# Kernel tuning notes

Hardware: AMD Instinct MI355X
Metric: run time of the kernel (lower is better)

Reference implementation:

```python
import jax, jax.numpy as jnp
import numpy as np

N = 50000      # nodes
E = 800000     # edges (avg degree 16)
LM = 768       # lm_input_dim
H = 192        # hidden_dim = 32*6
B6 = 32        # per-branch dim = hidden_dim/6
SLOPE = 0.01   # nn.LeakyReLU default negative slope


def setup_inputs() -> dict:
    key = jax.random.key(0)
    ks = jax.random.split(key, 32)
    f = lambda i, shape, s=0.05: (jax.random.normal(ks[i], shape, jnp.float32) * s)
    inp = {
        "pre_x": f(0, (N, LM)),
        "x": f(1, (N, LM)),
        "edge_index": jax.random.randint(ks[2], (2, E), 0, N),
        "edge_type": jax.random.randint(ks[3], (E,), 0, 3),
        "num_prop": f(4, (N, 5)),
        "num_category": f(5, (N, 1)),
        "des_tensor": f(6, (N, LM)),
        "tweet_tensor": f(7, (N, LM)),
        # parameters (torch nn.Linear convention: W is [out, in], y = x @ W.T + b)
        "W_des": f(8, (B6, LM)), "b_des": f(9, (B6,)),
        "W_tweet": f(10, (B6, LM)), "b_tweet": f(11, (B6,)),
        "W_tweet_tr": f(12, (B6, LM)), "b_tweet_tr": f(13, (B6,)),
        "W_prop": f(14, (B6, 5)), "b_prop": f(15, (B6,)),
        "W_cat": f(16, (B6, 1)), "b_cat": f(17, (B6,)),
        "W_text": f(18, (B6, LM)), "b_text": f(19, (B6,)),
        "W_in": f(20, (H, H)), "b_in": f(21, (H,)),
        "W_c1": f(22, (H, H)), "b_c1": f(23, (H,)),
        "W_c2": f(24, (H, H)), "b_c2": f(25, (H,)),
        "W_o1": f(26, (96, H)), "b_o1": f(27, (96,)),
        "W_o2": f(28, (2, 96)), "b_o2": f(29, (2,)),
    }
    return inp


def _gcn_conv(h, W, b, src, dst):
    """PyG GCNConv: symmetric-normalized aggregation with added self-loops.
    out[v] = sum_{u->v} (d_u d_v)^{-1/2} (h_u W^T) + (1/d_v) (h_v W^T) + b
    where d includes the self-loop (+1)."""
    n = h.shape[0]
    hW = h @ W.T                                                  # [N, H]
    deg = jax.ops.segment_sum(jnp.ones(src.shape[0], h.dtype), dst,
                              num_segments=n) + 1.0               # [N]
    dinv = jax.lax.rsqrt(deg)
    norm = dinv[src] * dinv[dst]                                  # [E]
    agg = jax.ops.segment_sum(hW[src] * norm[:, None], dst,
                              num_segments=n)                     # [N, H]
    return agg + hW * (1.0 / deg)[:, None] + b


def reference(pre_x, x, edge_index, edge_type, num_prop, num_category,
              des_tensor, tweet_tensor,
              W_des, b_des, W_tweet, b_tweet, W_tweet_tr, b_tweet_tr,
              W_prop, b_prop, W_cat, b_cat, W_text, b_text,
              W_in, b_in, W_c1, b_c1, W_c2, b_c2,
              W_o1, b_o1, W_o2, b_o2):
    lrelu = lambda v: jax.nn.leaky_relu(v, SLOPE)
    branch = lambda t, W, b: lrelu(t @ W.T + b)   # dropout is identity in eval

    d = branch(des_tensor, W_des, b_des)
    pre_t = branch(pre_x, W_tweet, b_tweet)
    t = branch(x, W_tweet_tr, b_tweet_tr)
    n = branch(num_prop, W_prop, b_prop)
    c = branch(num_category, W_cat, b_cat)
    tw = branch(tweet_tensor, W_text, b_text)

    h = jnp.concatenate((n, c, d, tw, pre_t, t), axis=1)          # [N, 192]
    h = lrelu(h @ W_in.T + b_in)

    src, dst = edge_index[0], edge_index[1]
    h = _gcn_conv(h, W_c1, b_c1, src, dst)
    h = _gcn_conv(h, W_c2, b_c2, src, dst)

    em = lrelu(h @ W_o1.T + b_o1)                                 # [N, 96]
    out = em @ W_o2.T + b_o2                                      # [N, 2]
    return (out, em)
```

## Files before the change

### kernel.cpp

```cpp
#include <hip/hip_runtime.h>

#define NN 50000
#define EE 800000
#define LMD 768
#define HD 192
#define SLOPE 0.01f

typedef short bf16x8 __attribute__((ext_vector_type(8)));
typedef float f32x4 __attribute__((ext_vector_type(4)));
typedef unsigned short u16;

__device__ __forceinline__ float lrelu(float v){ return v > 0.f ? v : SLOPE * v; }

__device__ __forceinline__ u16 f2bf(float f){
    unsigned u = __float_as_uint(f);
    u += 0x7FFF + ((u >> 16) & 1u);
    return (u16)(u >> 16);
}
__device__ __forceinline__ float bf2f(u16 v){
    return __uint_as_float(((unsigned)v) << 16);
}
__device__ __forceinline__ bf16x8 as_bf8(float4 v){
    union { float4 f; bf16x8 b; } u; u.f = v; return u.b;
}

__global__ __launch_bounds__(256) void k_prep(
    const float* __restrict__ W0, const float* __restrict__ W1,
    const float* __restrict__ W2, const float* __restrict__ W3,
    const float* __restrict__ Win, const float* __restrict__ Wc1,
    const float* __restrict__ Wc2, const float* __restrict__ Wo1,
    u16* __restrict__ out)
{
    int m = blockIdx.y;
    int idx = blockIdx.x * 256 + threadIdx.x;
    const float* src; int nelem; int K;
    switch (m) {
      case 0: src = W0;  nelem = 32*768;  K = 768; break;
      case 1: src = W1;  nelem = 32*768;  K = 768; break;
      case 2: src = W2;  nelem = 32*768;  K = 768; break;
      case 3: src = W3;  nelem = 32*768;  K = 768; break;
      case 4: src = Win; nelem = 192*192; K = 192; break;
      case 5: src = Wc1; nelem = 192*192; K = 192; break;
      case 6: src = Wc2; nelem = 192*192; K = 192; break;
      default: src = Wo1; nelem = 96*192; K = 192; break;
    }
    if (idx >= nelem) return;
    u16 v = f2bf(src[idx]);
    int c = idx / K, k = idx - c * K;
    int cb = c >> 4, lr = c & 15;
    int sg = k >> 5, kk = k & 31, hi = kk >> 3, j = kk & 7;
    int lane = hi * 16 + lr;
    size_t dst;
    if (m < 4)      dst = (size_t)m * 24576 + (sg * 2 + cb) * 512 + lane * 8 + j;
    else if (m < 7) dst = 98304 + (size_t)(m - 4) * 36864 + (sg * 12 + cb) * 512 + lane * 8 + j;
    else            dst = 208896 + (size_t)(sg * 6 + cb) * 512 + lane * 8 + j;
    out[dst] = v;
}

__global__ __launch_bounds__(256, 3) void k_branch(
    const float* __restrict__ des, const float* __restrict__ twt,
    const float* __restrict__ prex, const float* __restrict__ xx,
    const u16* __restrict__ Wf,
    const float* __restrict__ bd, const float* __restrict__ btx,
    const float* __restrict__ btw, const float* __restrict__ btr,
    u16* __restrict__ h)
{
    __shared__ u16 Abuf[16][776];
    __shared__ float scr[4][16][32];

    const int br = blockIdx.y;
    const float* A; const float* bias; int colBase;
    switch (br) {
      case 0:  A = des;  bias = bd;  colBase = 64;  break;
      case 1:  A = twt;  bias = btx; colBase = 96;  break;
      case 2:  A = prex; bias = btw; colBase = 128; break;
      default: A = xx;   bias = btr; colBase = 160; break;
    }

    const int t0 = threadIdx.x, w = t0 >> 6, l = t0 & 63;
    const int hi = l >> 4, lr = l & 15;

    bf16x8 Bfr[12];
    {
        const u16* wp = Wf + br * 24576;
        #pragma unroll
        for (int cc = 0; cc < 6; ++cc)
            #pragma unroll
            for (int cb = 0; cb < 2; ++cb)
                Bfr[cc * 2 + cb] = *(const bf16x8*)(wp + ((w * 6 + cc) * 2 + cb) * 512 + l * 8);
    }

    const int rrow = t0 >> 4;
    const int col0 = (t0 & 15) * 2;
    const float bias0 = bias[col0], bias1 = bias[col0 + 1];

    float4 f4[12];
    int tile = blockIdx.x;
    {
        const float* ab = A + (size_t)tile * 12288 + w * 3072 + l * 4;
        #pragma unroll
        for (int i = 0; i < 12; ++i) f4[i] = *(const float4*)(ab + i * 256);
    }

    for (; tile < 3125; tile += 192) {
        asm volatile("s_waitcnt vmcnt(0)" ::: "memory");
        #pragma unroll
        for (int i = 0; i < 12; ++i) {
            const int rr = i / 3, third = i % 3;
            uint2 pk;
            pk.x = (unsigned)f2bf(f4[i].x) | ((unsigned)f2bf(f4[i].y) << 16);
            pk.y = (unsigned)f2bf(f4[i].z) | ((unsigned)f2bf(f4[i].w) << 16);
            *(uint2*)&Abuf[w * 4 + rr][third * 256 + l * 4] = pk;
        }
        const int tnext = tile + 192;
        if (tnext < 3125) {
            const float* ab = A + (size_t)tnext * 12288 + w * 3072 + l * 4;
            #pragma unroll
            for (int i = 0; i < 12; ++i) f4[i] = *(const float4*)(ab + i * 256);
        }
        __syncthreads();

        f32x4 acc[2] = {};
        #pragma unroll
        for (int cc = 0; cc < 6; ++cc) {
            const int cg = w * 6 + cc;
            bf16x8 af = *(const bf16x8*)&Abuf[lr][cg * 32 + hi * 8];
            acc[0] = __builtin_amdgcn_mfma_f32_16x16x32_bf16(af, Bfr[cc * 2 + 0], acc[0], 0, 0, 0);
            acc[1] = __builtin_amdgcn_mfma_f32_16x16x32_bf16(af, Bfr[cc * 2 + 1], acc[1], 0, 0, 0);
        }
        #pragma unroll
        for (int cb = 0; cb < 2; ++cb)
            #pragma unroll
            for (int rg = 0; rg < 4; ++rg)
                scr[w][hi * 4 + rg][cb * 16 + lr] = acc[cb][rg];
        __syncthreads();

        float2 s; s.x = 0.f; s.y = 0.f;
        #pragma unroll
        for (int ww = 0; ww < 4; ++ww) {
            float2 p = *(const float2*)&scr[ww][rrow][col0];
            s.x += p.x; s.y += p.y;
        }
        unsigned pk = (unsigned)f2bf(lrelu(s.x + bias0)) | ((unsigned)f2bf(lrelu(s.y + bias1)) << 16);
        *(unsigned*)&h[((size_t)tile * 16 + rrow) * HD + colBase + col0] = pk;
    }
}

__global__ __launch_bounds__(256) void k_small_branch(
    const float* __restrict__ nprop, const float* __restrict__ ncat,
    const float* __restrict__ Wp, const float* __restrict__ bp,
    const float* __restrict__ Wc, const float* __restrict__ bc,
    u16* __restrict__ h)
{
    __shared__ float sWp[160], sbp[32], sWc[32], sbc[32];
    int t = threadIdx.x;
    if (t < 160) sWp[t] = Wp[t];
    else if (t < 192) sbp[t - 160] = bp[t - 160];
    else if (t < 224) sWc[t - 192] = Wc[t - 192];
    else              sbc[t - 224] = bc[t - 224];
    __syncthreads();

    int idx = blockIdx.x * 256 + t;
    if (idx >= NN * 8) return;
    int row = idx >> 3, g = idx & 7;
    float o[8];
    if (g < 4) {
        float np[5];
        #pragma unroll
        for (int k = 0; k < 5; ++k) np[k] = nprop[row * 5 + k];
        #pragma unroll
        for (int j = 0; j < 8; ++j) {
            int c = g * 8 + j;
            float a = sbp[c];
            #pragma unroll
            for (int k = 0; k < 5; ++k) a += np[k] * sWp[c * 5 + k];
            o[j] = lrelu(a);
        }
    } else {
        float nc = ncat[row];
        #pragma unroll
        for (int j = 0; j < 8; ++j) {
            int cc = (g - 4) * 8 + j;
            o[j] = lrelu(sbc[cc] + nc * sWc[cc]);
        }
    }
    uint4 pk;
    pk.x = (unsigned)f2bf(o[0]) | ((unsigned)f2bf(o[1]) << 16);
    pk.y = (unsigned)f2bf(o[2]) | ((unsigned)f2bf(o[3]) << 16);
    pk.z = (unsigned)f2bf(o[4]) | ((unsigned)f2bf(o[5]) << 16);
    pk.w = (unsigned)f2bf(o[6]) | ((unsigned)f2bf(o[7]) << 16);
    *(uint4*)&h[(size_t)row * HD + g * 8] = pk;
}

template<bool BIAS, bool LRELU>
__global__ __launch_bounds__(512) void k_hgemm(
    const u16* __restrict__ A, const u16* __restrict__ Wf,
    const float* __restrict__ bias, u16* __restrict__ out)
{
    __shared__ u16 Bs[36864];
    const int t = threadIdx.x, w = t >> 6, l = t & 63;
    const int hi = l >> 4, lr = l & 15;
    const int rowBase = blockIdx.x * 128;
    {
        const uint4* s_ = (const uint4*)Wf; uint4* d_ = (uint4*)Bs;
        #pragma unroll
        for (int i = 0; i < 9; ++i) d_[i * 512 + t] = s_[i * 512 + t];
    }
    int r0 = rowBase + w * 16 + lr;
    int rowc = r0 < NN ? r0 : NN - 1;
    const u16* ap = A + (size_t)rowc * HD;
    float4 araw[6];
    #pragma unroll
    for (int sg = 0; sg < 6; ++sg) {
        araw[sg] = *(const float4*)(ap + sg * 32 + hi * 8);
        asm volatile("" :: "v"(araw[sg].x), "v"(araw[sg].y), "v"(araw[sg].z), "v"(araw[sg].w));
    }
    __syncthreads();

    f32x4 acc[12] = {};
    #pragma unroll
    for (int sg = 0; sg < 6; ++sg) {
        bf16x8 af = as_bf8(araw[sg]);
        #pragma unroll
        for (int cb = 0; cb < 12; ++cb) {
            bf16x8 bf = *(const bf16x8*)(Bs + (sg * 12 + cb) * 512 + l * 8);
            acc[cb] = __builtin_amdgcn_mfma_f32_16x16x32_bf16(af, bf, acc[cb], 0, 0, 0);
        }
    }

    #pragma unroll
    for (int cb = 0; cb < 12; ++cb) {
        int cl = cb * 16 + lr;
        float bv = BIAS ? bias[cl] : 0.f;
        #pragma unroll
        for (int rg = 0; rg < 4; ++rg) {
            int r = rowBase + w * 16 + hi * 4 + rg;
            if (r < NN) {
                float v = acc[cb][rg] + bv;
                if (LRELU) v = lrelu(v);
                out[(size_t)r * HD + cl] = f2bf(v);
            }
        }
    }
}

__global__ __launch_bounds__(512) void k_final(
    const u16* __restrict__ A, const u16* __restrict__ Wf,
    const float* __restrict__ b1, const float* __restrict__ W2,
    const float* __restrict__ b2, float* __restrict__ em, float* __restrict__ out)
{
    __shared__ u16 Bs[18432];
    const int t = threadIdx.x, w = t >> 6, l = t & 63;
    const int hi = l >> 4, lr = l & 15;
    const int rowBase = blockIdx.x * 128;
    {
        const uint4* s_ = (const uint4*)Wf; uint4* d_ = (uint4*)Bs;
        #pragma unroll
        for (int i = 0; i < 5; ++i) { int idx = i * 512 + t; if (idx < 2304) d_[idx] = s_[idx]; }
    }
    int r0 = rowBase + w * 16 + lr;
    int rowc = r0 < NN ? r0 : NN - 1;
    const u16* ap = A + (size_t)rowc * HD;
    float4 araw[6];
    #pragma unroll
    for (int sg = 0; sg < 6; ++sg) {
        araw[sg] = *(const float4*)(ap + sg * 32 + hi * 8);
        asm volatile("" :: "v"(araw[sg].x), "v"(araw[sg].y), "v"(araw[sg].z), "v"(araw[sg].w));
    }
    __syncthreads();

    f32x4 acc[6] = {};
    #pragma unroll
    for (int sg = 0; sg < 6; ++sg) {
        bf16x8 af = as_bf8(araw[sg]);
        #pragma unroll
        for (int cb = 0; cb < 6; ++cb) {
            bf16x8 bf = *(const bf16x8*)(Bs + (sg * 6 + cb) * 512 + l * 8);
            acc[cb] = __builtin_amdgcn_mfma_f32_16x16x32_bf16(af, bf, acc[cb], 0, 0, 0);
        }
    }

    float w2v[2][6], bv[6];
    #pragma unroll
    for (int cb = 0; cb < 6; ++cb) {
        bv[cb] = b1[cb * 16 + lr];
        w2v[0][cb] = W2[cb * 16 + lr];
        w2v[1][cb] = W2[96 + cb * 16 + lr];
    }

    #pragma unroll
    for (int rg = 0; rg < 4; ++rg) {
        int r = rowBase + w * 16 + hi * 4 + rg;
        float o0 = 0.f, o1 = 0.f;
        #pragma unroll
        for (int cb = 0; cb < 6; ++cb) {
            float v = lrelu(acc[cb][rg] + bv[cb]);
            if (r < NN) em[(size_t)r * 96 + cb * 16 + lr] = v;
            o0 += v * w2v[0][cb];
            o1 += v * w2v[1][cb];
        }
        #pragma unroll
        for (int d = 1; d < 16; d <<= 1) {
            o0 += __shfl_xor(o0, d);
            o1 += __shfl_xor(o1, d);
        }
        if (lr == 0 && r < NN) {
            out[r * 2 + 0] = o0 + b2[0];
            out[r * 2 + 1] = o1 + b2[1];
        }
    }
}

__global__ void k_count(const int* __restrict__ ei, int* __restrict__ deg)
{
    int e = blockIdx.x * 256 + threadIdx.x;
    if (e < EE) atomicAdd(&deg[ei[EE + e]], 1);
}

__global__ __launch_bounds__(1024) void k_scan1(const int* __restrict__ deg, int* __restrict__ rp,
                                                int* __restrict__ part,
                                                float* __restrict__ dinv, float* __restrict__ invdeg)
{
    __shared__ int sh[1024];
    int tid = threadIdx.x, i = blockIdx.x * 1024 + tid;
    int x = (i < NN) ? deg[i] : 0;
    if (i < NN) {
        float d = (float)(x + 1);
        dinv[i] = rsqrtf(d);
        invdeg[i] = 1.0f / d;
    }
    sh[tid] = x;
    __syncthreads();
    for (int off = 1; off < 1024; off <<= 1) {
        int y = (tid >= off) ? sh[tid - off] : 0;
        __syncthreads();
        sh[tid] += y;
        __syncthreads();
    }
    if (i < NN) rp[i] = sh[tid] - x;
    if (tid == 1023) part[blockIdx.x] = sh[tid];
}

__global__ void k_scan3(const int* __restrict__ deg, int* __restrict__ rp,
                        const int* __restrict__ part, int* __restrict__ cursor)
{
    int i = blockIdx.x * 256 + threadIdx.x;
    int pb = blockIdx.x >> 2;
    int pre = 0;
    for (int j = 0; j < pb; ++j) pre += part[j];
    if (i < NN) {
        int v = rp[i] + pre;
        rp[i] = v;
        cursor[i] = v;
        if (i == NN - 1) rp[NN] = v + deg[i];
    }
}

__global__ void k_fill(const int* __restrict__ ei, const float* __restrict__ dinv,
                       int* __restrict__ cursor, int* __restrict__ cs, float* __restrict__ nrm)
{
    int e = blockIdx.x * 256 + threadIdx.x;
    if (e >= EE) return;
    int s = ei[e], d = ei[EE + e];
    int pos = atomicAdd(&cursor[d], 1);
    cs[pos] = s;
    nrm[pos] = dinv[s] * dinv[d];
}

__global__ __launch_bounds__(256) void k_agg(const u16* __restrict__ hW,
    const int* __restrict__ rp, const int* __restrict__ cs, const float* __restrict__ nrm,
    const float* __restrict__ invdeg, const float* __restrict__ bias, u16* __restrict__ out)
{
    int lane = threadIdx.x;
    if (lane >= 48) return;
    int v = blockIdx.x * 4 + threadIdx.y;
    int f0 = lane * 4;
    int s0 = rp[v], s1 = rp[v + 1];
    float4 bv = *reinterpret_cast<const float4*>(bias + f0);
    ushort4 hv = *reinterpret_cast<const ushort4*>(hW + (size_t)v * HD + f0);
    float idg = invdeg[v];
    float a0 = bf2f(hv.x) * idg + bv.x;
    float a1 = bf2f(hv.y) * idg + bv.y;
    float a2 = bf2f(hv.z) * idg + bv.z;
    float a3 = bf2f(hv.w) * idg + bv.w;
    int i = s0;
    for (; i + 8 <= s1; i += 8) {
        int c[8]; float n[8]; ushort4 g[8];
        #pragma unroll
        for (int j = 0; j < 8; ++j) { c[j] = cs[i + j]; n[j] = nrm[i + j]; }
        #pragma unroll
        for (int j = 0; j < 8; ++j)
            g[j] = *reinterpret_cast<const ushort4*>(hW + (size_t)c[j] * HD + f0);
        #pragma unroll
        for (int j = 0; j < 8; ++j) {
            a0 += bf2f(g[j].x) * n[j]; a1 += bf2f(g[j].y) * n[j];
            a2 += bf2f(g[j].z) * n[j]; a3 += bf2f(g[j].w) * n[j];
        }
    }
    for (; i < s1; ++i) {
        int c = cs[i]; float n = nrm[i];
        ushort4 g = *reinterpret_cast<const ushort4*>(hW + (size_t)c * HD + f0);
        a0 += bf2f(g.x) * n; a1 += bf2f(g.y) * n; a2 += bf2f(g.z) * n; a3 += bf2f(g.w) * n;
    }
    ushort4 o;
    o.x = f2bf(a0); o.y = f2bf(a1); o.z = f2bf(a2); o.w = f2bf(a3);
    *reinterpret_cast<ushort4*>(out + (size_t)v * HD + f0) = o;
}

extern "C" void kernel_launch(void* const* d_in, const int* in_sizes, int n_in,
                              void* d_out, int out_size, void* d_ws, size_t ws_size,
                              hipStream_t stream)
{
    const float* pre_x = (const float*)d_in[0];
    const float* x     = (const float*)d_in[1];
    const int*   ei    = (const int*)d_in[2];
    const float* nprop = (const float*)d_in[4];
    const float* ncat  = (const float*)d_in[5];
    const float* des   = (const float*)d_in[6];
    const float* twt   = (const float*)d_in[7];
    const float* W_des  = (const float*)d_in[8],  *b_des  = (const float*)d_in[9];
    const float* W_tw   = (const float*)d_in[10], *b_tw   = (const float*)d_in[11];
    const float* W_tr   = (const float*)d_in[12], *b_tr   = (const float*)d_in[13];
    const float* W_prop = (const float*)d_in[14], *b_prop = (const float*)d_in[15];
    const float* W_cat  = (const float*)d_in[16], *b_cat  = (const float*)d_in[17];
    const float* W_text = (const float*)d_in[18], *b_text = (const float*)d_in[19];
    const float* W_in   = (const float*)d_in[20], *b_in   = (const float*)d_in[21];
    const float* W_c1   = (const float*)d_in[22], *b_c1   = (const float*)d_in[23];
    const float* W_c2   = (const float*)d_in[24], *b_c2   = (const float*)d_in[25];
    const float* W_o1   = (const float*)d_in[26], *b_o1   = (const float*)d_in[27];
    const float* W_o2   = (const float*)d_in[28], *b_o2   = (const float*)d_in[29];

    char* base = (char*)d_ws;
    size_t off = 0;
    auto alloc = [&](size_t bytes) -> char* {
        char* p = base + off;
        off = (off + bytes + 255) & ~(size_t)255;
        return p;
    };
    u16*   hA     = (u16*)alloc((size_t)NN * HD * 2);
    u16*   hB     = (u16*)alloc((size_t)NN * HD * 2);
    u16*   hC     = (u16*)alloc((size_t)NN * HD * 2);
    u16*   Wprep  = (u16*)alloc((size_t)227328 * 2);
    float* dinv   = (float*)alloc((size_t)NN * 4);
    float* invdeg = (float*)alloc((size_t)NN * 4);
    int*   deg    = (int*)alloc((size_t)NN * 4);
    int*   rp     = (int*)alloc((size_t)(NN + 1) * 4);
    int*   cursor = (int*)alloc((size_t)NN * 4);
    int*   part   = (int*)alloc(64 * 4);
    int*   cs     = (int*)alloc((size_t)EE * 4);
    float* nrm    = (float*)alloc((size_t)EE * 4);
    (void)ws_size; (void)in_sizes; (void)n_in; (void)out_size;

    float* outp = (float*)d_out;
    float* em   = outp + (size_t)NN * 2;

    const int rb     = (NN + 255) / 256;
    const int rb128  = (NN + 127) / 128;
    const int eb     = (EE + 255) / 256;
    const int nb1024 = (NN + 1023) / 1024;

    hipMemsetAsync(deg, 0, (size_t)NN * 4, stream);
    hipLaunchKernelGGL(k_prep, dim3(144, 8), dim3(256), 0, stream,
        W_des, W_text, W_tw, W_tr, W_in, W_c1, W_c2, W_o1, Wprep);
    hipLaunchKernelGGL(k_count,  dim3(eb), dim3(256), 0, stream, ei, deg);
    hipLaunchKernelGGL(k_scan1,  dim3(nb1024), dim3(1024), 0, stream, deg, rp, part, dinv, invdeg);
    hipLaunchKernelGGL(k_scan3,  dim3(rb), dim3(256), 0, stream, deg, rp, part, cursor);
    hipLaunchKernelGGL(k_fill,   dim3(eb), dim3(256), 0, stream, ei, dinv, cursor, cs, nrm);

    hipLaunchKernelGGL(k_branch, dim3(192, 4), dim3(256), 0, stream,
        des, twt, pre_x, x, Wprep, b_des, b_text, b_tw, b_tr, hA);
    hipLaunchKernelGGL(k_small_branch, dim3((NN * 8 + 255) / 256), dim3(256), 0, stream,
        nprop, ncat, W_prop, b_prop, W_cat, b_cat, hA);

    hipLaunchKernelGGL((k_hgemm<true, true>),   dim3(rb128), dim3(512), 0, stream,
        hA, Wprep + 98304, b_in, hB);
    hipLaunchKernelGGL((k_hgemm<false, false>), dim3(rb128), dim3(512), 0, stream,
        hB, Wprep + 98304 + 36864, nullptr, hC);
    hipLaunchKernelGGL(k_agg, dim3(NN / 4), dim3(64, 4), 0, stream, hC, rp, cs, nrm, invdeg, b_c1, hB);
    hipLaunchKernelGGL((k_hgemm<false, false>), dim3(rb128), dim3(512), 0, stream,
        hB, Wprep + 98304 + 2 * 36864, nullptr, hC);
    hipLaunchKernelGGL(k_agg, dim3(NN / 4), dim3(64, 4), 0, stream, hC, rp, cs, nrm, invdeg, b_c2, hB);

    hipLaunchKernelGGL(k_final, dim3(rb128), dim3(512), 0, stream,
        hB, Wprep + 208896, b_o1, W_o2, b_o2, em, outp);
}
```

Baseline: 400.8 us.

## Fold CSR graph build into compute kernels as extra blocks

The separate degree-count, scan and fill kernels are removed, and their work is given to extra blocks appended to the branch GEMM, the small-branch kernel and the first two hidden GEMMs. Graph preprocessing therefore runs alongside dense compute with fewer kernel launches. The branch GEMM also switches from strided tile assignment to contiguous tile ranges per block. In exchange, the scan uses 256-wide partials with a serial prefix over up to 196 parts, and the atomic-heavy blocks compete with the GEMM blocks for compute units.

```diff
diff --git a/kernel.cpp b/kernel.cpp
--- a/kernel.cpp
+++ b/kernel.cpp
@@ -63,10 +63,18 @@
     const u16* __restrict__ Wf,
     const float* __restrict__ bd, const float* __restrict__ btx,
     const float* __restrict__ btw, const float* __restrict__ btr,
-    u16* __restrict__ h)
+    u16* __restrict__ h,
+    const int* __restrict__ ei, int* __restrict__ deg)
 {
     __shared__ u16 Abuf[16][776];
     __shared__ float scr[4][16][32];
+
+    if (blockIdx.x >= 192) {
+        int rid = blockIdx.y * 64 + (blockIdx.x - 192);
+        for (int e = rid * 256 + threadIdx.x; e < EE; e += 65536)
+            atomicAdd(&deg[ei[EE + e]], 1);
+        return;
+    }
 
     const int br = blockIdx.y;
     const float* A; const float* bias; int colBase;
@@ -94,15 +102,18 @@
     const int col0 = (t0 & 15) * 2;
     const float bias0 = bias[col0], bias1 = bias[col0 + 1];
 
+    const int b = blockIdx.x;
+    const int nt = (b < 53) ? 17 : 16;
+    int tile = b * 16 + (b < 53 ? b : 53);
+
     float4 f4[12];
-    int tile = blockIdx.x;
     {
         const float* ab = A + (size_t)tile * 12288 + w * 3072 + l * 4;
         #pragma unroll
         for (int i = 0; i < 12; ++i) f4[i] = *(const float4*)(ab + i * 256);
     }
 
-    for (; tile < 3125; tile += 192) {
+    for (int it = 0; it < nt; ++it, ++tile) {
         asm volatile("s_waitcnt vmcnt(0)" ::: "memory");
         #pragma unroll
         for (int i = 0; i < 12; ++i) {
@@ -112,9 +123,8 @@
             pk.y = (unsigned)f2bf(f4[i].z) | ((unsigned)f2bf(f4[i].w) << 16);
             *(uint2*)&Abuf[w * 4 + rr][third * 256 + l * 4] = pk;
         }
-        const int tnext = tile + 192;
-        if (tnext < 3125) {
-            const float* ab = A + (size_t)tnext * 12288 + w * 3072 + l * 4;
+        if (it + 1 < nt) {
+            const float* ab = A + (size_t)(tile + 1) * 12288 + w * 3072 + l * 4;
             #pragma unroll
             for (int i = 0; i < 12; ++i) f4[i] = *(const float4*)(ab + i * 256);
         }
@@ -146,12 +156,38 @@
     }
 }
 
-__global__ __launch_bounds__(256) void k_small_branch(
+__global__ __launch_bounds__(256) void k_small_scan(
     const float* __restrict__ nprop, const float* __restrict__ ncat,
     const float* __restrict__ Wp, const float* __restrict__ bp,
     const float* __restrict__ Wc, const float* __restrict__ bc,
-    u16* __restrict__ h)
-{
+    u16* __restrict__ h,
+    const int* __restrict__ deg, int* __restrict__ rp, int* __restrict__ part,
+    float* __restrict__ dinv, float* __restrict__ invdeg)
+{
+    if (blockIdx.x >= 1563) {
+        __shared__ int sh[256];
+        int sb = blockIdx.x - 1563;
+        int tid = threadIdx.x;
+        int i = sb * 256 + tid;
+        int x = (i < NN) ? deg[i] : 0;
+        if (i < NN) {
+            float d = (float)(x + 1);
+            dinv[i] = rsqrtf(d);
+            invdeg[i] = 1.0f / d;
+        }
+        sh[tid] = x;
+        __syncthreads();
+        for (int off = 1; off < 256; off <<= 1) {
+            int y = (tid >= off) ? sh[tid - off] : 0;
+            __syncthreads();
+            sh[tid] += y;
+            __syncthreads();
+        }
+        if (i < NN) rp[i] = sh[tid] - x;
+        if (tid == 255) part[sb] = sh[255];
+        return;
+    }
+
     __shared__ float sWp[160], sbp[32], sWc[32], sbc[32];
     int t = threadIdx.x;
     if (t < 160) sWp[t] = Wp[t];
@@ -192,12 +228,42 @@
     *(uint4*)&h[(size_t)row * HD + g * 8] = pk;
 }
 
-template<bool BIAS, bool LRELU>
+template<bool BIAS, bool LRELU, int ROLE>
 __global__ __launch_bounds__(512) void k_hgemm(
     const u16* __restrict__ A, const u16* __restrict__ Wf,
-    const float* __restrict__ bias, u16* __restrict__ out)
+    const float* __restrict__ bias, u16* __restrict__ out,
+    const int* __restrict__ deg, int* __restrict__ rp, const int* __restrict__ part,
+    int* __restrict__ cursor, const int* __restrict__ ei,
+    int* __restrict__ cs, float* __restrict__ nrm, const float* __restrict__ dinv)
 {
     __shared__ u16 Bs[36864];
+    if (ROLE == 1 && blockIdx.x >= 391) {
+        int sb = blockIdx.x - 391;
+        int tid = threadIdx.x;
+        if (tid < 256) {
+            int pre = 0;
+            for (int j = 0; j < sb; ++j) pre += part[j];
+            int i = sb * 256 + tid;
+            if (i < NN) {
+                int v = rp[i] + pre;
+                rp[i] = v;
+                cursor[i] = v;
+                if (i == NN - 1) rp[NN] = v + deg[i];
+            }
+        }
+        return;
+    }
+    if (ROLE == 2 && blockIdx.x >= 391) {
+        int rid = blockIdx.x - 391;
+        for (int e = rid * 512 + threadIdx.x; e < EE; e += 102400) {
+            int s = ei[e], d = ei[EE + e];
+            int pos = atomicAdd(&cursor[d], 1);
+            cs[pos] = s;
+            nrm[pos] = dinv[s] * dinv[d];
+        }
+        return;
+    }
+
     const int t = threadIdx.x, w = t >> 6, l = t & 63;
     const int hi = l >> 4, lr = l & 15;
     const int rowBase = blockIdx.x * 128;
@@ -309,62 +375,6 @@
             out[r * 2 + 1] = o1 + b2[1];
         }
     }
-}
-
-__global__ void k_count(const int* __restrict__ ei, int* __restrict__ deg)
-{
-    int e = blockIdx.x * 256 + threadIdx.x;
-    if (e < EE) atomicAdd(&deg[ei[EE + e]], 1);
-}
-
-__global__ __launch_bounds__(1024) void k_scan1(const int* __restrict__ deg, int* __restrict__ rp,
-                                                int* __restrict__ part,
-                                                float* __restrict__ dinv, float* __restrict__ invdeg)
-{
-    __shared__ int sh[1024];
-    int tid = threadIdx.x, i = blockIdx.x * 1024 + tid;
-    int x = (i < NN) ? deg[i] : 0;
-    if (i < NN) {
-        float d = (float)(x + 1);
-        dinv[i] = rsqrtf(d);
-        invdeg[i] = 1.0f / d;
-    }
-    sh[tid] = x;
-    __syncthreads();
-    for (int off = 1; off < 1024; off <<= 1) {
-        int y = (tid >= off) ? sh[tid - off] : 0;
-        __syncthreads();
-        sh[tid] += y;
-        __syncthreads();
-    }
-    if (i < NN) rp[i] = sh[tid] - x;
-    if (tid == 1023) part[blockIdx.x] = sh[tid];
-}
-
-__global__ void k_scan3(const int* __restrict__ deg, int* __restrict__ rp,
-                        const int* __restrict__ part, int* __restrict__ cursor)
-{
-    int i = blockIdx.x * 256 + threadIdx.x;
-    int pb = blockIdx.x >> 2;
-    int pre = 0;
-    for (int j = 0; j < pb; ++j) pre += part[j];
-    if (i < NN) {
-        int v = rp[i] + pre;
-        rp[i] = v;
-        cursor[i] = v;
-        if (i == NN - 1) rp[NN] = v + deg[i];
-    }
-}
-
-__global__ void k_fill(const int* __restrict__ ei, const float* __restrict__ dinv,
-                       int* __restrict__ cursor, int* __restrict__ cs, float* __restrict__ nrm)
-{
-    int e = blockIdx.x * 256 + threadIdx.x;
-    if (e >= EE) return;
-    int s = ei[e], d = ei[EE + e];
-    int pos = atomicAdd(&cursor[d], 1);
-    cs[pos] = s;
-    nrm[pos] = dinv[s] * dinv[d];
 }
 
 __global__ __launch_bounds__(256) void k_agg(const u16* __restrict__ hW,
@@ -446,7 +456,7 @@
     int*   deg    = (int*)alloc((size_t)NN * 4);
     int*   rp     = (int*)alloc((size_t)(NN + 1) * 4);
     int*   cursor = (int*)alloc((size_t)NN * 4);
-    int*   part   = (int*)alloc(64 * 4);
+    int*   part   = (int*)alloc(256 * 4);
     int*   cs     = (int*)alloc((size_t)EE * 4);
     float* nrm    = (float*)alloc((size_t)EE * 4);
     (void)ws_size; (void)in_sizes; (void)n_in; (void)out_size;
@@ -454,33 +464,35 @@
     float* outp = (float*)d_out;
     float* em   = outp + (size_t)NN * 2;
 
-    const int rb     = (NN + 255) / 256;
-    const int rb128  = (NN + 127) / 128;
-    const int eb     = (EE + 255) / 256;
-    const int nb1024 = (NN + 1023) / 1024;
-
     hipMemsetAsync(deg, 0, (size_t)NN * 4, stream);
     hipLaunchKernelGGL(k_prep, dim3(144, 8), dim3(256), 0, stream,
         W_des, W_text, W_tw, W_tr, W_in, W_c1, W_c2, W_o1, Wprep);
-    hipLaunchKernelGGL(k_count,  dim3(eb), dim3(256), 0, stream, ei, deg);
-    hipLaunchKernelGGL(k_scan1,  dim3(nb1024), dim3(1024), 0, stream, deg, rp, part, dinv, invdeg);
-    hipLaunchKernelGGL(k_scan3,  dim3(rb), dim3(256), 0, stream, deg, rp, part, cursor);
-    hipLaunchKernelGGL(k_fill,   dim3(eb), dim3(256), 0, stream, ei, dinv, cursor, cs, nrm);
-
-    hipLaunchKernelGGL(k_branch, dim3(192, 4), dim3(256), 0, stream,
-        des, twt, pre_x, x, Wprep, b_des, b_text, b_tw, b_tr, hA);
-    hipLaunchKernelGGL(k_small_branch, dim3((NN * 8 + 255) / 256), dim3(256), 0, stream,
-        nprop, ncat, W_prop, b_prop, W_cat, b_cat, hA);
-
-    hipLaunchKernelGGL((k_hgemm<true, true>),   dim3(rb128), dim3(512), 0, stream,
-        hA, Wprep + 98304, b_in, hB);
-    hipLaunchKernelGGL((k_hgemm<false, false>), dim3(rb128), dim3(512), 0, stream,
-        hB, Wprep + 98304 + 36864, nullptr, hC);
-    hipLaunchKernelGGL(k_agg, dim3(NN / 4), dim3(64, 4), 0, stream, hC, rp, cs, nrm, invdeg, b_c1, hB);
-    hipLaunchKernelGGL((k_hgemm<false, false>), dim3(rb128), dim3(512), 0, stream,
-        hB, Wprep + 98304 + 2 * 36864, nullptr, hC);
-    hipLaunchKernelGGL(k_agg, dim3(NN / 4), dim3(64, 4), 0, stream, hC, rp, cs, nrm, invdeg, b_c2, hB);
-
-    hipLaunchKernelGGL(k_final, dim3(rb128), dim3(512), 0, stream,
+
+    hipLaunchKernelGGL(k_branch, dim3(256, 4), dim3(256), 0, stream,
+        des, twt, pre_x, x, Wprep, b_des, b_text, b_tw, b_tr, hA, ei, deg);
+
+    hipLaunchKernelGGL(k_small_scan, dim3(1759), dim3(256), 0, stream,
+        nprop, ncat, W_prop, b_prop, W_cat, b_cat, hA,
+        deg, rp, part, dinv, invdeg);
+
+    hipLaunchKernelGGL((k_hgemm<true, true, 1>), dim3(587), dim3(512), 0, stream,
+        hA, Wprep + 98304, b_in, hB,
+        deg, rp, part, cursor, ei, cs, nrm, dinv);
+
+    hipLaunchKernelGGL((k_hgemm<false, false, 2>), dim3(591), dim3(512), 0, stream,
+        hB, Wprep + 98304 + 36864, nullptr, hC,
+        deg, rp, part, cursor, ei, cs, nrm, dinv);
+
+    hipLaunchKernelGGL(k_agg, dim3(NN / 4), dim3(64, 4), 0, stream,
+        hC, rp, cs, nrm, invdeg, b_c1, hB);
+
+    hipLaunchKernelGGL((k_hgemm<false, false, 0>), dim3(391), dim3(512), 0, stream,
+        hB, Wprep + 98304 + 2 * 36864, nullptr, hC,
+        deg, rp, part, cursor, ei, cs, nrm, dinv);
+
+    hipLaunchKernelGGL(k_agg, dim3(NN / 4), dim3(64, 4), 0, stream,
+        hC, rp, cs, nrm, invdeg, b_c2, hB);
+
+    hipLaunchKernelGGL(k_final, dim3(391), dim3(512), 0, stream,
         hB, Wprep + 208896, b_o1, W_o2, b_o2, em, outp);
 }
```

After: 376.9 us. 1.06x faster.
